# Kernel optimization log

Hardware: AMD Instinct MI355X
Metric: run time of the kernel (lower is better)

The kernel has to match this reference:

```python
import jax, jax.numpy as jnp
import numpy as np

MUL = 64          # multiplicity of every irrep block
EMB = 64

# --- normalize_function(gelu): scale phi so E[phi(N(0,1))^2] = 1 (e3nn convention) ---
_z = np.linspace(-8.0, 8.0, 4001)
_gauss = np.exp(-0.5 * _z**2) / np.sqrt(2.0 * np.pi)
_PHI_C = float(np.sqrt(np.trapz(np.asarray(jax.nn.gelu(jnp.asarray(_z)))**2 * _gauss, _z)))

# Levi-Civita tensor (real Wigner 3j for 1x1->1 up to normalization)
_eps = np.zeros((3, 3, 3), np.float32)
for (i, j, k), s in {(0,1,2):1,(1,2,0):1,(2,0,1):1,(0,2,1):-1,(2,1,0):-1,(1,0,2):-1}.items():
    _eps[i, j, k] = s
EPS = jnp.asarray(_eps)

INV_SQ3 = 1.0 / np.sqrt(3.0)   # w3j(1,1,0) component (after sqrt(2l3+1) component-norm scaling)
INV_SQ2 = 1.0 / np.sqrt(2.0)   # eps/sqrt(6) * sqrt(3)
ALPHA_01 = 1.0 / np.sqrt(2.0 * MUL * MUL)  # two uvw paths feed outputs 0e and 1o
ALPHA_2  = 1.0 / np.sqrt(1.0 * MUL * MUL)  # one path feeds 1e


def _mlp(x, Ws):
    # haiku Linear(no bias, N(0,1) init), x -> phi(x @ W / sqrt(fan_in)) with normalized phi
    for W in Ws:
        x = jax.nn.gelu(x @ W * (x.shape[-1] ** -0.5)) / _PHI_C
    return x


def setup_inputs() -> dict:
    key = jax.random.key(0)
    ks = jax.random.split(key, 11)
    B = 128
    return {
        "emb": jax.random.normal(ks[0], (B, EMB), jnp.float32),
        "x1": jax.random.normal(ks[1], (B, 4 * MUL), jnp.float32),   # 64x0e + 64x1o
        "x2": jax.random.normal(ks[2], (B, 4 * MUL), jnp.float32),
        "W0": jax.random.normal(ks[3], (EMB, 256), jnp.float32),
        "W1": jax.random.normal(ks[4], (256, 256), jnp.float32),
        "W2": jax.random.normal(ks[5], (256, 64), jnp.float32),
        "P0": jax.random.normal(ks[6], (64, MUL, MUL, MUL), jnp.float32),
        "P1": jax.random.normal(ks[7], (64, MUL, MUL, MUL), jnp.float32),
        "P2": jax.random.normal(ks[8], (64, MUL, MUL, MUL), jnp.float32),
        "P3": jax.random.normal(ks[9], (64, MUL, MUL, MUL), jnp.float32),
        "P4": jax.random.normal(ks[10], (64, MUL, MUL, MUL), jnp.float32),
    }


def reference(emb, x1, x2, W0, W1, W2, P0, P1, P2, P3, P4):
    B = emb.shape[0]
    # MLP -> per-sample weight vector h  [B, 64]
    h = _mlp(emb, (W0, W1, W2))
    hs = h * (h.shape[-1] ** -0.5)  # / sqrt(w.shape[0])
    # per-instruction generated path weights  [B, u, v, w]
    w0, w1, w2, w3, w4 = (jnp.einsum('xuvw,bx->buvw', P, hs) for P in (P0, P1, P2, P3, P4))

    s1, v1 = x1[:, :MUL], x1[:, MUL:].reshape(B, MUL, 3)
    s2, v2 = x2[:, :MUL], x2[:, MUL:].reshape(B, MUL, 3)

    # (0e,0e)->0e and (1o,1o)->0e
    t0 = jnp.einsum('bu,bv,buvw->bw', s1, s2, w0)
    t3 = jnp.einsum('bui,bvi,buvw->bw', v1, v2, w3) * INV_SQ3
    out0 = ALPHA_01 * (t0 + t3)                      # [B, MUL]
    # (0e,1o)->1o and (1o,0e)->1o
    t1 = jnp.einsum('bu,bvj,buvw->bwj', s1, v2, w1)
    t2 = jnp.einsum('bui,bv,buvw->bwi', v1, s2, w2)
    out1 = ALPHA_01 * (t1 + t2)                      # [B, MUL, 3]
    # (1o,1o)->1e  (cross-product path)
    t4 = jnp.einsum('bui,bvj,buvw,ijk->bwk', v1, v2, w4, EPS) * INV_SQ2
    out2 = ALPHA_2 * t4                              # [B, MUL, 3]

    return jnp.concatenate([out0, out1.reshape(B, 3 * MUL), out2.reshape(B, 3 * MUL)], axis=-1)
```

## Files before the change

kernel.cpp:

```cpp
#include <hip/hip_runtime.h>

typedef float v4f __attribute__((ext_vector_type(4)));
typedef short v8s __attribute__((ext_vector_type(8)));

__device__ __forceinline__ unsigned short f2bf_rn(float f) {
  unsigned u = __float_as_uint(f);
  return (unsigned short)((u + 0x7fffu + ((u >> 16) & 1u)) >> 16);
}
__device__ __forceinline__ float bf2f(unsigned short h) {
  return __uint_as_float((unsigned)h << 16);
}

__device__ __forceinline__ float gelu_phi(float x) {
  float t = tanhf(0.7978845608f * (x + 0.044715f * x * x * x));
  return 0.5f * x * (1.0f + t) * 1.5338375f;
}

__global__ __launch_bounds__(256) void k_mlp1(const float* __restrict__ emb, const float* __restrict__ W0,
                                              const float* __restrict__ x1, const float* __restrict__ x2,
                                              float* __restrict__ act1,
                                              unsigned short* __restrict__ s1c, unsigned short* __restrict__ v1c,
                                              unsigned short* __restrict__ s2c, unsigned short* __restrict__ v2c)
{
  const int blk = blockIdx.x, tid = threadIdx.x;
  if (blk < 128) {
    float s = 0.f;
#pragma unroll 8
    for (int xx = 0; xx < 64; ++xx) s += emb[blk * 64 + xx] * W0[xx * 256 + tid];
    act1[blk * 256 + tid] = gelu_phi(s * 0.125f);
  } else {
    const int sel = (blk - 128) >> 3;
    const float* xs = sel ? x2 : x1;
    unsigned short* sc = sel ? s2c : s1c;
    unsigned short* vc = sel ? v2c : v1c;
    for (int i = ((blk - 128) & 7) * 256 + tid; i < 32768; i += 2048) {
      if (i < 8192) {
        sc[i] = f2bf_rn(xs[(i >> 6) * 256 + (i & 63)]);
      } else {
        const int t = i - 8192, g = t >> 13, r = t & 8191;
        vc[g * 8192 + r] = f2bf_rn(xs[(r >> 6) * 256 + 64 + (r & 63) * 3 + g]);
      }
    }
  }
}

__global__ __launch_bounds__(256) void k_mlp2(const float* __restrict__ act1, const float* __restrict__ W1,
                                              float* __restrict__ act2)
{
  const int b = blockIdx.x, j = threadIdx.x;
  float s = 0.f;
#pragma unroll 16
  for (int x = 0; x < 256; ++x) s += act1[b * 256 + x] * W1[x * 256 + j];
  act2[b * 256 + j] = gelu_phi(s * 0.0625f);
}

__global__ __launch_bounds__(256) void k_mlp3(const float* __restrict__ act2, const float* __restrict__ W2,
                                              float* __restrict__ hsT)
{
  const int o = blockIdx.x * 256 + threadIdx.x;
  const int b = o >> 6, e = o & 63;
  float s = 0.f;
#pragma unroll 16
  for (int x = 0; x < 256; ++x) s += act2[b * 256 + x] * W2[x * 64 + e];
  hsT[e * 128 + b] = gelu_phi(s * 0.0625f) * 0.125f;
}


template<int G>
__device__ __forceinline__ void gemm_body(
    const float* __restrict__ P,
    const unsigned short* __restrict__ f1g,
    const unsigned short* __restrict__ f2g,
    const float* __restrict__ hsT,
    float* __restrict__ partial,
    int c, int csh,
    unsigned short* ldsF1, unsigned* ldsB32)
{
  constexpr int NC  = (G == 0 || G == 3) ? 1 : 3;
  constexpr int NF2 = (G == 0 || G == 2) ? 1 : 3;
  constexpr int NH  = (G == 0 || G == 1) ? 1 : 3;
  constexpr int NCM = (G <= 1) ? 1 : 3;
  constexpr int RB  = (G == 0) ? 0 : (G == 1) ? 128 : (G == 2) ? 512 : (G == 3) ? 896 : 1024;

  const int tid = threadIdx.x;
  const int lane = tid & 63, w = tid >> 6, l16 = lane & 15, quad = lane >> 4;
  const int tq = tid & 15, kp = tid >> 4;
  const int x = c >> (csh - 6);
  const int nsub = 1 << (7 - csh);

  int bidx[2];
  bidx[0] = w * 32 + l16;
  bidx[1] = w * 32 + 16 + l16;

  float hsx[2];
  hsx[0] = hsT[x * 128 + bidx[0]];
  hsx[1] = hsT[x * 128 + bidx[1]];

  v8s fr2[2][NF2][2];
#pragma unroll
  for (int bh = 0; bh < 2; ++bh)
#pragma unroll
    for (int m = 0; m < NF2; ++m)
#pragma unroll
      for (int h = 0; h < 2; ++h)
        fr2[bh][m][h] = *(const v8s*)(f2g + m * 8192 + bidx[bh] * 64 + h * 32 + quad * 8);

  v4f acc[2][NC][4];
#pragma unroll
  for (int bh = 0; bh < 2; ++bh)
#pragma unroll
    for (int cc = 0; cc < NC; ++cc)
#pragma unroll
      for (int nf = 0; nf < 4; ++nf) acc[bh][cc][nf] = (v4f){0.f, 0.f, 0.f, 0.f};

  const int swz_w = (tq & 3) << 2;
  const int swz_r = ((l16 >> 2) & 3) << 2;

  float h[2][NH];

  for (int sub = 0; sub < nsub; ++sub) {
    const int kb = (c << (18 - csh)) + (sub << 11);
    const int u0 = (kb >> 6) & 63;
    __syncthreads();
    {
      const int nchk = NCM * 512;
      for (int i = tid; i < nchk; i += 256) {
        const int uu8 = i & 3, b = (i >> 2) & 127, cm = i >> 9;
        *(v8s*)&ldsF1[(cm * 128 + b) * 40 + uu8 * 8] =
            *(const v8s*)(f1g + cm * 8192 + b * 64 + u0 + uu8 * 8);
      }
    }

    auto gload = [&](int kk, float4& r0, float4& r1) {
      const float* s = P + (size_t)(kb + kk * 32 + 2 * kp) * 64 + 4 * tq;
      r0 = *(const float4*)s;
      r1 = *(const float4*)(s + 64);
    };
    auto bwrite = [&](int buf, const float4& r0, const float4& r1) {
      unsigned* dst = ldsB32 + (size_t)(buf * 64 + 4 * tq) * 20 + (kp ^ swz_w);
      dst[0]  = (unsigned)f2bf_rn(r0.x) | ((unsigned)f2bf_rn(r1.x) << 16);
      dst[20] = (unsigned)f2bf_rn(r0.y) | ((unsigned)f2bf_rn(r1.y) << 16);
      dst[40] = (unsigned)f2bf_rn(r0.z) | ((unsigned)f2bf_rn(r1.z) << 16);
      dst[60] = (unsigned)f2bf_rn(r0.w) | ((unsigned)f2bf_rn(r1.w) << 16);
    };

    float4 pa0, pa1;
    gload(0, pa0, pa1);
    bwrite(0, pa0, pa1);
    gload(1, pa0, pa1);
    __syncthreads();

#pragma unroll 2
    for (int kk = 0; kk < 64; ++kk) {
      const int buf = kk & 1;
      const int vh = kk & 1;
      v8s bfr[4];
#pragma unroll
      for (int nf = 0; nf < 4; ++nf)
        bfr[nf] = *(const v8s*)&ldsB32[(size_t)(buf * 64 + nf * 16 + l16) * 20 + ((quad * 4) ^ swz_r)];
      if (vh == 0) {
        const int uu = kk >> 1;
#pragma unroll
        for (int bh = 0; bh < 2; ++bh)
#pragma unroll
          for (int m = 0; m < NH; ++m)
            h[bh][m] = hsx[bh] * bf2f(ldsF1[m * 5120 + bidx[bh] * 40 + uu]);
      }
      if (kk < 63) bwrite(buf ^ 1, pa0, pa1);
      if (kk < 62) gload(kk + 2, pa0, pa1);
#pragma unroll
      for (int bh = 0; bh < 2; ++bh) {
#pragma unroll
        for (int cc = 0; cc < NC; ++cc) {
          v8s af;
#pragma unroll
          for (int j = 0; j < 8; ++j) {
            float p;
            if constexpr (G == 0)
              p = h[bh][0] * bf2f((unsigned short)fr2[bh][0][vh][j]);
            else if constexpr (G == 1)
              p = h[bh][0] * bf2f((unsigned short)fr2[bh][cc][vh][j]);
            else if constexpr (G == 2)
              p = h[bh][cc] * bf2f((unsigned short)fr2[bh][0][vh][j]);
            else if constexpr (G == 3)
              p = h[bh][0] * bf2f((unsigned short)fr2[bh][0][vh][j])
                + h[bh][1] * bf2f((unsigned short)fr2[bh][1][vh][j])
                + h[bh][2] * bf2f((unsigned short)fr2[bh][2][vh][j]);
            else {
              const int i1 = (cc + 1) % 3, j2 = (cc + 2) % 3;
              p = h[bh][i1] * bf2f((unsigned short)fr2[bh][j2][vh][j])
                - h[bh][j2] * bf2f((unsigned short)fr2[bh][i1][vh][j]);
            }
            af[j] = (short)(__float_as_uint(p) >> 16);
          }
#pragma unroll
          for (int nf = 0; nf < 4; ++nf)
            acc[bh][cc][nf] = __builtin_amdgcn_mfma_f32_16x16x32_bf16(af, bfr[nf], acc[bh][cc][nf], 0, 0, 0);
        }
      }
      __syncthreads();
    }
  }

#pragma unroll
  for (int bh = 0; bh < 2; ++bh)
#pragma unroll
    for (int cc = 0; cc < NC; ++cc)
#pragma unroll
      for (int nf = 0; nf < 4; ++nf)
#pragma unroll
        for (int r = 0; r < 4; ++r) {
          const int row = RB + cc * 128 + w * 32 + bh * 16 + quad * 4 + r;
          partial[((size_t)c * 1408 + row) * 64 + nf * 16 + l16] = acc[bh][cc][nf][r];
        }
}

__global__ __launch_bounds__(256, 2) void tp_gemm(
    const float* __restrict__ P0, const float* __restrict__ P1, const float* __restrict__ P2,
    const float* __restrict__ P3, const float* __restrict__ P4,
    const unsigned short* __restrict__ s1c, const unsigned short* __restrict__ v1c,
    const unsigned short* __restrict__ s2c, const unsigned short* __restrict__ v2c,
    const float* __restrict__ hsT, float* __restrict__ partial, int csh)
{
  __shared__ __align__(16) unsigned ldsB32[2 * 64 * 20];
  __shared__ __align__(16) unsigned short ldsF1[3 * 128 * 40];
  const int g = blockIdx.x >> csh;
  const int c = blockIdx.x & ((1 << csh) - 1);
  switch (g) {
    case 0: gemm_body<0>(P0, s1c, s2c, hsT, partial, c, csh, ldsF1, ldsB32); break;
    case 1: gemm_body<1>(P1, s1c, v2c, hsT, partial, c, csh, ldsF1, ldsB32); break;
    case 2: gemm_body<2>(P2, v1c, s2c, hsT, partial, c, csh, ldsF1, ldsB32); break;
    case 3: gemm_body<3>(P3, v1c, v2c, hsT, partial, c, csh, ldsF1, ldsB32); break;
    default: gemm_body<4>(P4, v1c, v2c, hsT, partial, c, csh, ldsF1, ldsB32); break;
  }
}

__global__ __launch_bounds__(448) void k_fin(const float* __restrict__ partial, float* __restrict__ out, int nch)
{
  const int b = blockIdx.x, i = threadIdx.x;
  int w, rA, rB;
  if (i < 64)       { w = i; rA = b; rB = 896 + b; }
  else if (i < 256) { const int t = i - 64;  w = t / 3; const int j = t - 3 * w; rA = 128 + j * 128 + b; rB = 512 + j * 128 + b; }
  else              { const int t = i - 256; w = t / 3; const int k = t - 3 * w; rA = 1024 + k * 128 + b; rB = rA; }
  const float* pA = partial + (size_t)rA * 64 + w;
  const float* pB = partial + (size_t)rB * 64 + w;
  float sA = 0.f, sB = 0.f;
#pragma unroll 4
  for (int cc = 0; cc < nch; ++cc) {
    sA += pA[(size_t)cc * 90112];
    sB += pB[(size_t)cc * 90112];
  }
  const float A01 = 0.011048543f;
  const float sc = 0.015625f * 0.70710678f;
  float o;
  if (i < 64)       o = A01 * (sA + 0.57735027f * sB);
  else if (i < 256) o = A01 * (sA + sB);
  else              o = sc * sA;
  out[b * 448 + i] = o;
}

extern "C" void kernel_launch(void* const* d_in, const int* in_sizes, int n_in,
                              void* d_out, int out_size, void* d_ws, size_t ws_size,
                              hipStream_t stream)
{
  const float* emb = (const float*)d_in[0];
  const float* x1  = (const float*)d_in[1];
  const float* x2  = (const float*)d_in[2];
  const float* W0  = (const float*)d_in[3];
  const float* W1  = (const float*)d_in[4];
  const float* W2  = (const float*)d_in[5];
  const float* P0  = (const float*)d_in[6];
  const float* P1  = (const float*)d_in[7];
  const float* P2  = (const float*)d_in[8];
  const float* P3  = (const float*)d_in[9];
  const float* P4  = (const float*)d_in[10];
  float* out = (float*)d_out;
  char* ws = (char*)d_ws;

  float* hsT = (float*)ws;
  unsigned short* s1c = (unsigned short*)(ws + 32768);
  unsigned short* v1c = (unsigned short*)(ws + 49152);
  unsigned short* s2c = (unsigned short*)(ws + 98304);
  unsigned short* v2c = (unsigned short*)(ws + 114688);
  float* act1 = (float*)(ws + 163840);
  float* act2 = (float*)(ws + 294912);
  float* partial = (float*)(ws + 163840);

  const int csh = (ws_size >= (size_t)163840 + ((size_t)360448 << 7)) ? 7 : 6;

  k_mlp1<<<144, 256, 0, stream>>>(emb, W0, x1, x2, act1, s1c, v1c, s2c, v2c);
  k_mlp2<<<128, 256, 0, stream>>>(act1, W1, act2);
  k_mlp3<<<32, 256, 0, stream>>>(act2, W2, hsT);
  tp_gemm<<<5 << csh, 256, 0, stream>>>(P0, P1, P2, P3, P4, s1c, v1c, s2c, v2c, hsT, partial, csh);
  k_fin<<<128, 448, 0, stream>>>(partial, out, 1 << csh);
}
```

Baseline: 398.5 us.

## Deepen P prefetch pipeline, use hardware bf16 pack, refine LDS swizzle

Replaces the single in-flight register pair for streamed P tiles with a rotating ring of NSET register sets (2 or 4 depending on the path). This keeps several global loads in flight ahead of the MFMA loop, with a peeled tail. The software float-to-bf16 rounding and truncation on both operands is replaced by the v_cvt_pk_bf16_f32 instruction, which also changes A-operand rounding from truncation to round-to-nearest. The LDS B-tile swizzle now also XORs in the fragment index to reduce bank conflicts, and the finalize reduction loop is unrolled further. More live registers could cut occupancy under the (256,2) launch bound.

New measurement: 730.6 us. 1.83x slower.

```diff
diff --git a/kernel.cpp b/kernel.cpp
--- a/kernel.cpp
+++ b/kernel.cpp
@@ -9,6 +9,11 @@
 }
 __device__ __forceinline__ float bf2f(unsigned short h) {
   return __uint_as_float((unsigned)h << 16);
+}
+__device__ __forceinline__ unsigned cvt_pk_bf16(float lo, float hi) {
+  unsigned r;
+  asm("v_cvt_pk_bf16_f32 %0, %1, %2" : "=v"(r) : "v"(lo), "v"(hi));
+  return r;
 }
 
 __device__ __forceinline__ float gelu_phi(float x) {
@@ -76,11 +81,12 @@
     int c, int csh,
     unsigned short* ldsF1, unsigned* ldsB32)
 {
-  constexpr int NC  = (G == 0 || G == 3) ? 1 : 3;
-  constexpr int NF2 = (G == 0 || G == 2) ? 1 : 3;
-  constexpr int NH  = (G == 0 || G == 1) ? 1 : 3;
-  constexpr int NCM = (G <= 1) ? 1 : 3;
-  constexpr int RB  = (G == 0) ? 0 : (G == 1) ? 128 : (G == 2) ? 512 : (G == 3) ? 896 : 1024;
+  constexpr int NC   = (G == 0 || G == 3) ? 1 : 3;
+  constexpr int NF2  = (G == 0 || G == 2) ? 1 : 3;
+  constexpr int NH   = (G == 0 || G == 1) ? 1 : 3;
+  constexpr int NCM  = (G <= 1) ? 1 : 3;
+  constexpr int RB   = (G == 0) ? 0 : (G == 1) ? 128 : (G == 2) ? 512 : (G == 3) ? 896 : 1024;
+  constexpr int NSET = (G == 1 || G == 4) ? 2 : 4;
 
   const int tid = threadIdx.x;
   const int lane = tid & 63, w = tid >> 6, l16 = lane & 15, quad = lane >> 4;
@@ -102,8 +108,8 @@
 #pragma unroll
     for (int m = 0; m < NF2; ++m)
 #pragma unroll
-      for (int h = 0; h < 2; ++h)
-        fr2[bh][m][h] = *(const v8s*)(f2g + m * 8192 + bidx[bh] * 64 + h * 32 + quad * 8);
+      for (int hh = 0; hh < 2; ++hh)
+        fr2[bh][m][hh] = *(const v8s*)(f2g + m * 8192 + bidx[bh] * 64 + hh * 32 + quad * 8);
 
   v4f acc[2][NC][4];
 #pragma unroll
@@ -113,8 +119,7 @@
 #pragma unroll
       for (int nf = 0; nf < 4; ++nf) acc[bh][cc][nf] = (v4f){0.f, 0.f, 0.f, 0.f};
 
-  const int swz_w = (tq & 3) << 2;
-  const int swz_r = ((l16 >> 2) & 3) << 2;
+  const int swz_w = (((tq & 3) ^ (tq >> 2)) << 2);
 
   float h[2][NH];
 
@@ -131,33 +136,27 @@
       }
     }
 
-    auto gload = [&](int kk, float4& r0, float4& r1) {
-      const float* s = P + (size_t)(kb + kk * 32 + 2 * kp) * 64 + 4 * tq;
-      r0 = *(const float4*)s;
-      r1 = *(const float4*)(s + 64);
+    float4 A0[NSET], A1[NSET];
+    auto gload = [&](int kk, int s) {
+      const float* p = P + (size_t)(kb + kk * 32 + 2 * kp) * 64 + 4 * tq;
+      A0[s] = *(const float4*)p;
+      A1[s] = *(const float4*)(p + 64);
     };
-    auto bwrite = [&](int buf, const float4& r0, const float4& r1) {
-      unsigned* dst = ldsB32 + (size_t)(buf * 64 + 4 * tq) * 20 + (kp ^ swz_w);
-      dst[0]  = (unsigned)f2bf_rn(r0.x) | ((unsigned)f2bf_rn(r1.x) << 16);
-      dst[20] = (unsigned)f2bf_rn(r0.y) | ((unsigned)f2bf_rn(r1.y) << 16);
-      dst[40] = (unsigned)f2bf_rn(r0.z) | ((unsigned)f2bf_rn(r1.z) << 16);
-      dst[60] = (unsigned)f2bf_rn(r0.w) | ((unsigned)f2bf_rn(r1.w) << 16);
+    auto bwrite = [&](int buf, int s) {
+      unsigned* dst = ldsB32 + (buf * 64 + 4 * tq) * 20 + (kp ^ swz_w);
+      dst[0]  = cvt_pk_bf16(A0[s].x, A1[s].x);
+      dst[20] = cvt_pk_bf16(A0[s].y, A1[s].y);
+      dst[40] = cvt_pk_bf16(A0[s].z, A1[s].z);
+      dst[60] = cvt_pk_bf16(A0[s].w, A1[s].w);
     };
 
-    float4 pa0, pa1;
-    gload(0, pa0, pa1);
-    bwrite(0, pa0, pa1);
-    gload(1, pa0, pa1);
-    __syncthreads();
-
-#pragma unroll 2
-    for (int kk = 0; kk < 64; ++kk) {
-      const int buf = kk & 1;
-      const int vh = kk & 1;
+    auto step = [&](int kk, bool wr, bool ld) {
+      const int buf = kk & 1, vh = kk & 1;
       v8s bfr[4];
 #pragma unroll
       for (int nf = 0; nf < 4; ++nf)
-        bfr[nf] = *(const v8s*)&ldsB32[(size_t)(buf * 64 + nf * 16 + l16) * 20 + ((quad * 4) ^ swz_r)];
+        bfr[nf] = *(const v8s*)&ldsB32[(buf * 64 + nf * 16 + l16) * 20 +
+                                       ((quad * 4) ^ ((((l16 >> 2) & 3) ^ nf) << 2))];
       if (vh == 0) {
         const int uu = kk >> 1;
 #pragma unroll
@@ -166,40 +165,54 @@
           for (int m = 0; m < NH; ++m)
             h[bh][m] = hsx[bh] * bf2f(ldsF1[m * 5120 + bidx[bh] * 40 + uu]);
       }
-      if (kk < 63) bwrite(buf ^ 1, pa0, pa1);
-      if (kk < 62) gload(kk + 2, pa0, pa1);
+      if (wr) bwrite(buf ^ 1, (kk + 1) & (NSET - 1));
+      if (ld) gload(kk + 1 + NSET, (kk + 1) & (NSET - 1));
+      auto pv = [&](int bh, int cc, int j) -> float {
+        if constexpr (G == 0)
+          return h[bh][0] * bf2f((unsigned short)fr2[bh][0][vh][j]);
+        else if constexpr (G == 1)
+          return h[bh][0] * bf2f((unsigned short)fr2[bh][cc][vh][j]);
+        else if constexpr (G == 2)
+          return h[bh][cc] * bf2f((unsigned short)fr2[bh][0][vh][j]);
+        else if constexpr (G == 3)
+          return h[bh][0] * bf2f((unsigned short)fr2[bh][0][vh][j])
+               + h[bh][1] * bf2f((unsigned short)fr2[bh][1][vh][j])
+               + h[bh][2] * bf2f((unsigned short)fr2[bh][2][vh][j]);
+        else {
+          const int i1 = (cc + 1) % 3, j2 = (cc + 2) % 3;
+          return h[bh][i1] * bf2f((unsigned short)fr2[bh][j2][vh][j])
+               - h[bh][j2] * bf2f((unsigned short)fr2[bh][i1][vh][j]);
+        }
+      };
 #pragma unroll
       for (int bh = 0; bh < 2; ++bh) {
 #pragma unroll
         for (int cc = 0; cc < NC; ++cc) {
           v8s af;
-#pragma unroll
-          for (int j = 0; j < 8; ++j) {
-            float p;
-            if constexpr (G == 0)
-              p = h[bh][0] * bf2f((unsigned short)fr2[bh][0][vh][j]);
-            else if constexpr (G == 1)
-              p = h[bh][0] * bf2f((unsigned short)fr2[bh][cc][vh][j]);
-            else if constexpr (G == 2)
-              p = h[bh][cc] * bf2f((unsigned short)fr2[bh][0][vh][j]);
-            else if constexpr (G == 3)
-              p = h[bh][0] * bf2f((unsigned short)fr2[bh][0][vh][j])
-                + h[bh][1] * bf2f((unsigned short)fr2[bh][1][vh][j])
-                + h[bh][2] * bf2f((unsigned short)fr2[bh][2][vh][j]);
-            else {
-              const int i1 = (cc + 1) % 3, j2 = (cc + 2) % 3;
-              p = h[bh][i1] * bf2f((unsigned short)fr2[bh][j2][vh][j])
-                - h[bh][j2] * bf2f((unsigned short)fr2[bh][i1][vh][j]);
-            }
-            af[j] = (short)(__float_as_uint(p) >> 16);
-          }
+          unsigned* a32 = (unsigned*)&af;
+#pragma unroll
+          for (int t = 0; t < 4; ++t)
+            a32[t] = cvt_pk_bf16(pv(bh, cc, 2 * t), pv(bh, cc, 2 * t + 1));
 #pragma unroll
           for (int nf = 0; nf < 4; ++nf)
             acc[bh][cc][nf] = __builtin_amdgcn_mfma_f32_16x16x32_bf16(af, bfr[nf], acc[bh][cc][nf], 0, 0, 0);
         }
       }
       __syncthreads();
+    };
+
+#pragma unroll
+    for (int s = 0; s < NSET; ++s) gload(s, s);
+    bwrite(0, 0);
+    gload(NSET, 0);
+    __syncthreads();
+
+    for (int k4 = 0; k4 < 56; k4 += 4) {
+#pragma unroll
+      for (int i = 0; i < 4; ++i) step(k4 + i, true, true);
     }
+#pragma unroll
+    for (int i = 0; i < 8; ++i) step(56 + i, i < 7, i < 7 - NSET);
   }
 
 #pragma unroll
@@ -245,7 +258,7 @@
   const float* pA = partial + (size_t)rA * 64 + w;
   const float* pB = partial + (size_t)rB * 64 + w;
   float sA = 0.f, sB = 0.f;
-#pragma unroll 4
+#pragma unroll 8
   for (int cc = 0; cc < nch; ++cc) {
     sA += pA[(size_t)cc * 90112];
     sB += pB[(size_t)cc * 90112];
```
